# Performance work log

Hardware: AMD Instinct MI355X
Metric: run time of the kernel (lower is better)

The kernel has to match this reference:

```python
import jax, jax.numpy as jnp
import numpy as np
import math

D_MODEL = 1024
NUM_HEADS = 16
HEAD_DIM = D_MODEL // NUM_HEADS  # 64


def setup_inputs() -> dict:
    key = jax.random.key(0)
    ks = jax.random.split(key, 5)
    B, T = 4, 2048
    scale = 1.0 / math.sqrt(D_MODEL)
    return {
        "x": jax.random.normal(ks[0], (B, T, D_MODEL), dtype=jnp.float32),
        "wq": jax.random.normal(ks[1], (D_MODEL, D_MODEL), dtype=jnp.float32) * scale,
        "wk": jax.random.normal(ks[2], (D_MODEL, D_MODEL), dtype=jnp.float32) * scale,
        "wv": jax.random.normal(ks[3], (D_MODEL, D_MODEL), dtype=jnp.float32) * scale,
        "wo": jax.random.normal(ks[4], (D_MODEL, D_MODEL), dtype=jnp.float32) * scale,
    }


def reference(x, wq, wk, wv, wo):
    B, T, _ = x.shape
    H, Dk = NUM_HEADS, HEAD_DIM

    def split_heads(t):  # [B,T,D] -> [B,H,T,Dk]
        return t.reshape(B, T, H, Dk).transpose(0, 2, 1, 3)

    q = split_heads(x @ wq)
    k = split_heads(x @ wk)
    v = split_heads(x @ wv)

    # scaled QK^T: [B,H,T,T]
    scores = jnp.einsum("bhqd,bhkd->bhqk", q, k) / jnp.sqrt(jnp.float32(Dk))
    # causal mask: triu(ones, diag=0).T.bool() == lower-triangular incl. diagonal
    causal = jnp.tril(jnp.ones((T, T), dtype=bool))
    scores = jnp.where(causal, scores, -jnp.inf)
    attn = jax.nn.softmax(scores, axis=-1)

    out = jnp.einsum("bhqk,bhkd->bhqd", attn, v)  # [B,H,T,Dk]
    out = out.transpose(0, 2, 1, 3).reshape(B, T, H * Dk)
    return out @ wo
```

## Files before the change

kernel.cpp:

```cpp
#include <hip/hip_runtime.h>
#include <hip/hip_bf16.h>
#include <stdint.h>

typedef __attribute__((ext_vector_type(8))) short bf16x8;
typedef __attribute__((ext_vector_type(4))) float f32x4;
typedef __attribute__((ext_vector_type(4))) unsigned short u16x4;
typedef __attribute__((ext_vector_type(4))) float float4v;

#define MFMA16(a, b, c) __builtin_amdgcn_mfma_f32_16x16x32_bf16((a), (b), (c), 0, 0, 0)

__device__ __forceinline__ unsigned short f2bf(float f) {
  return __builtin_bit_cast(unsigned short, (__bf16)f);
}
__device__ __forceinline__ float m3(float a, float b, float c) {
  return fmaxf(fmaxf(a, b), c);
}

typedef const __attribute__((address_space(1))) void* gptr1_t;
typedef __attribute__((address_space(3))) void* lptr3_t;
__device__ __forceinline__ void gload16(const void* g, void* l) {
  __builtin_amdgcn_global_load_lds((gptr1_t)g, (lptr3_t)l, 16, 0, 0);
}

__global__ __launch_bounds__(256) void cvt_x_kernel(const float* __restrict__ in,
                                                    unsigned short* __restrict__ out) {
  int i = blockIdx.x * 256 + threadIdx.x;
  float4v f = ((const float4v*)in)[i];
  u16x4 o;
  o[0] = f2bf(f[0]); o[1] = f2bf(f[1]); o[2] = f2bf(f[2]); o[3] = f2bf(f[3]);
  ((u16x4*)out)[i] = o;
}

__global__ __launch_bounds__(256) void wt_cvt_kernel(const float* __restrict__ w0,
                                                     const float* __restrict__ w1,
                                                     const float* __restrict__ w2,
                                                     const float* __restrict__ w3,
                                                     unsigned short* __restrict__ out) {
  const float* in = blockIdx.z == 0 ? w0 : blockIdx.z == 1 ? w1 : blockIdx.z == 2 ? w2 : w3;
  unsigned short* o = out + (size_t)blockIdx.z * 1024 * 1024;
  __shared__ float tile[32][33];
  int tx = threadIdx.x & 31, ty = threadIdx.x >> 5;
  int c0 = blockIdx.x * 32, r0 = blockIdx.y * 32;
#pragma unroll
  for (int i = 0; i < 4; i++)
    tile[ty + 8 * i][tx] = in[(size_t)(r0 + ty + 8 * i) * 1024 + c0 + tx];
  __syncthreads();
#pragma unroll
  for (int i = 0; i < 4; i++)
    o[(size_t)(c0 + ty + 8 * i) * 1024 + r0 + tx] = f2bf(tile[tx][ty + 8 * i]);
}

template <bool OUTF32>
__global__ __launch_bounds__(256) void gemm128_kernel(
    const unsigned short* __restrict__ A,
    const unsigned short* __restrict__ B0, const unsigned short* __restrict__ B1,
    const unsigned short* __restrict__ B2,
    void* C0, void* C1, void* C2) {
  constexpr int K = 1024, N = 1024;
  const unsigned short* Bt = blockIdx.z == 0 ? B0 : blockIdx.z == 1 ? B1 : B2;
  void* Cv = blockIdx.z == 0 ? C0 : blockIdx.z == 1 ? C1 : C2;

  __shared__ unsigned short As[128 * 32];
  __shared__ unsigned short Bs[128 * 32];

  const int tid = threadIdx.x;
  const int w = tid >> 6, lane = tid & 63, l15 = lane & 15, l4 = lane >> 4;
  const int wm = w >> 1, wn = w & 1;
  const int m0 = blockIdx.x * 128, n0 = blockIdx.y * 128;

  f32x4 acc[4][4] = {};

  const int srow = w * 32 + (lane >> 2);
  const int scol = (lane & 3) * 8;
  const unsigned short* ga = A + (size_t)(m0 + srow) * K + scol;
  const unsigned short* gb = Bt + (size_t)(n0 + srow) * K + scol;
  char* lA = (char*)As + w * 2048;
  char* lB = (char*)Bs + w * 2048;

  for (int k0 = 0; k0 < K; k0 += 32) {
    __syncthreads();
    gload16(ga + k0, lA);
    gload16(ga + k0 + 16 * K, lA + 1024);
    gload16(gb + k0, lB);
    gload16(gb + k0 + 16 * K, lB + 1024);
    __syncthreads();

    bf16x8 af[4], bfr[4];
#pragma unroll
    for (int mi = 0; mi < 4; mi++)
      af[mi] = *(const bf16x8*)&As[(wm * 64 + mi * 16 + l15) * 32 + 8 * l4];
#pragma unroll
    for (int ni = 0; ni < 4; ni++)
      bfr[ni] = *(const bf16x8*)&Bs[(wn * 64 + ni * 16 + l15) * 32 + 8 * l4];
#pragma unroll
    for (int mi = 0; mi < 4; mi++)
#pragma unroll
      for (int ni = 0; ni < 4; ni++)
        acc[mi][ni] = MFMA16(af[mi], bfr[ni], acc[mi][ni]);
  }

#pragma unroll
  for (int mi = 0; mi < 4; mi++)
#pragma unroll
    for (int ni = 0; ni < 4; ni++)
#pragma unroll
      for (int r = 0; r < 4; r++) {
        int mg = m0 + wm * 64 + mi * 16 + 4 * l4 + r;
        int ng = n0 + wn * 64 + ni * 16 + l15;
        if (OUTF32)
          ((float*)Cv)[(size_t)mg * N + ng] = acc[mi][ni][r];
        else
          ((unsigned short*)Cv)[(size_t)mg * N + ng] = f2bf(acc[mi][ni][r]);
      }
}

__global__ __launch_bounds__(256) void gemm64_kernel(const unsigned short* __restrict__ A,
                                                     const unsigned short* __restrict__ Bt,
                                                     float* __restrict__ Cv) {
  constexpr int K = 1024, N = 1024;
  __shared__ unsigned short As[64 * 32];
  __shared__ unsigned short Bs[128 * 32];

  const int tid = threadIdx.x;
  const int w = tid >> 6, lane = tid & 63, l15 = lane & 15, l4 = lane >> 4;
  const int wm = w >> 1, wn = w & 1;
  const int m0 = blockIdx.x * 64, n0 = blockIdx.y * 128;

  f32x4 acc[2][4] = {};

  const int arow = w * 16 + (lane >> 2);
  const int brow = w * 32 + (lane >> 2);
  const int scol = (lane & 3) * 8;
  const unsigned short* ga = A + (size_t)(m0 + arow) * K + scol;
  const unsigned short* gb = Bt + (size_t)(n0 + brow) * K + scol;
  char* lA = (char*)As + w * 1024;
  char* lB = (char*)Bs + w * 2048;

  for (int k0 = 0; k0 < K; k0 += 32) {
    __syncthreads();
    gload16(ga + k0, lA);
    gload16(gb + k0, lB);
    gload16(gb + k0 + 16 * K, lB + 1024);
    __syncthreads();

    bf16x8 af[2], bfr[4];
#pragma unroll
    for (int mi = 0; mi < 2; mi++)
      af[mi] = *(const bf16x8*)&As[(wm * 32 + mi * 16 + l15) * 32 + 8 * l4];
#pragma unroll
    for (int ni = 0; ni < 4; ni++)
      bfr[ni] = *(const bf16x8*)&Bs[(wn * 64 + ni * 16 + l15) * 32 + 8 * l4];
#pragma unroll
    for (int mi = 0; mi < 2; mi++)
#pragma unroll
      for (int ni = 0; ni < 4; ni++)
        acc[mi][ni] = MFMA16(af[mi], bfr[ni], acc[mi][ni]);
  }

#pragma unroll
  for (int mi = 0; mi < 2; mi++)
#pragma unroll
    for (int ni = 0; ni < 4; ni++)
#pragma unroll
      for (int r = 0; r < 4; r++) {
        int mg = m0 + wm * 32 + mi * 16 + 4 * l4 + r;
        int ng = n0 + wn * 64 + ni * 16 + l15;
        Cv[(size_t)mg * N + ng] = acc[mi][ni][r];
      }
}

__global__ __launch_bounds__(256, 4) void attn_kernel(const unsigned short* __restrict__ Qb,
                                                      const unsigned short* __restrict__ Kb,
                                                      const unsigned short* __restrict__ Vb,
                                                      unsigned short* __restrict__ Ob) {
  const int bid = blockIdx.x;
  const int xcd = bid & 7, slot = bid >> 3;
  const int hb = xcd * 8 + (slot >> 4);
  const int p = slot & 15;
  const int h = hb & 15, bb = hb >> 4;

  const int tid = threadIdx.x, w = tid >> 6, lane = tid & 63, l15 = lane & 15, l4 = lane >> 4;

  __shared__ unsigned short K_lds[2][64 * 64];
  __shared__ unsigned short Vt_lds[2][64 * 64];
  __shared__ unsigned short P_lds[4][16 * 64];

  const size_t brow = (size_t)bb * 2048;
  const int qq = w * 16 + l15;
  const int sw = 8 * (l15 & 7);
  constexpr float C = 0.18033688f;
  const bf16x8 ones = {0x3F80, 0x3F80, 0x3F80, 0x3F80, 0x3F80, 0x3F80, 0x3F80, 0x3F80};

  const int qbA = p, qbB = 31 - p;
  const int lastB = qbB;

  bf16x8 qfA0, qfA1, qfB0, qfB1;
  {
    const unsigned short* qa = Qb + (brow + qbA * 64 + qq) * 1024 + h * 64 + 8 * l4;
    qfA0 = *(const bf16x8*)qa;
    qfA1 = *(const bf16x8*)(qa + 32);
    const unsigned short* qbp = Qb + (brow + qbB * 64 + qq) * 1024 + h * 64 + 8 * l4;
    qfB0 = *(const bf16x8*)qbp;
    qfB1 = *(const bf16x8*)(qbp + 32);
  }

  f32x4 oA[4] = {}, oB[4] = {};
  f32x4 lA4 = {0.f, 0.f, 0.f, 0.f}, lB4 = {0.f, 0.f, 0.f, 0.f};
  float mrA = -__builtin_inff(), mrB = -__builtin_inff();

  const int kcol = 8 * ((lane & 7) ^ ((lane >> 3) & 7));
  const unsigned short* gk = Kb + (brow + 8 * w + (lane >> 3)) * 1024 + h * 64 + kcol;
  const int vr0 = 2 * (tid >> 3);
  const int vsc = (tid & 7) * 8;
  const unsigned short* gv = Vb + (brow + vr0) * 1024 + h * 64 + vsc;

  auto vt_write = [&](int buf, const bf16x8& v0, const bf16x8& v1) {
#pragma unroll
    for (int j = 0; j < 8; j++) {
      const int d = vsc + j;
      const int msk = 8 * ((d ^ (d >> 3)) & 7);
      uint32_t pk = (uint32_t)(unsigned short)v0[j] |
                    ((uint32_t)(unsigned short)v1[j] << 16);
      *(uint32_t*)&Vt_lds[buf][d * 64 + (vr0 ^ msk)] = pk;
    }
  };

  auto tile_compute = [&](const unsigned short* Kc, const unsigned short* Vtc,
                          const bf16x8& q0f, const bf16x8& q1f, f32x4* oacc,
                          float& m_run, f32x4& lacc, bool diag) {
    f32x4 s[4];
    __builtin_amdgcn_s_setprio(1);
#pragma unroll
    for (int sub = 0; sub < 4; ++sub) {
      const unsigned short* kr0 = &Kc[(sub * 16 + l15) * 64 + ((8 * l4) ^ sw)];
      const unsigned short* kr1 = &Kc[(sub * 16 + l15) * 64 + ((32 + 8 * l4) ^ sw)];
      f32x4 z = {0.f, 0.f, 0.f, 0.f};
      z = MFMA16(*(const bf16x8*)kr0, q0f, z);
      z = MFMA16(*(const bf16x8*)kr1, q1f, z);
      s[sub] = z;
    }
    __builtin_amdgcn_s_setprio(0);

    if (diag) {
#pragma unroll
      for (int sub = 0; sub < 4; ++sub)
#pragma unroll
        for (int r4 = 0; r4 < 4; r4++) {
          const int kv_t = sub * 16 + 4 * l4 + r4;
          s[sub][r4] = (kv_t > qq) ? -__builtin_inff() : s[sub][r4];
        }
    }
    const float t0 = m3(s[0][0], s[0][1], s[0][2]);
    const float t1 = m3(s[0][3], s[1][0], s[1][1]);
    const float t2 = m3(s[1][2], s[1][3], s[2][0]);
    const float t3 = m3(s[2][1], s[2][2], s[2][3]);
    const float t4 = m3(s[3][0], s[3][1], s[3][2]);
    float mt = fmaxf(m3(t0, t1, t2), m3(t3, t4, s[3][3]));
    mt = fmaxf(mt, __shfl_xor(mt, 16));
    mt = fmaxf(mt, __shfl_xor(mt, 32));

    if (!__all(mt <= m_run + 44.3614f)) {
      const float m_new = fmaxf(m_run, mt);
      const float alpha = __builtin_amdgcn_exp2f((m_run - m_new) * C);
      const float ao0 = __shfl(alpha, 4 * l4 + 0);
      const float ao1 = __shfl(alpha, 4 * l4 + 1);
      const float ao2 = __shfl(alpha, 4 * l4 + 2);
      const float ao3 = __shfl(alpha, 4 * l4 + 3);
#pragma unroll
      for (int d = 0; d < 4; ++d) {
        oacc[d][0] *= ao0; oacc[d][1] *= ao1; oacc[d][2] *= ao2; oacc[d][3] *= ao3;
      }
      lacc[0] *= ao0; lacc[1] *= ao1; lacc[2] *= ao2; lacc[3] *= ao3;
      m_run = m_new;
    }
    const float mnc = m_run * C;

#pragma unroll
    for (int sub = 0; sub < 4; ++sub) {
      u16x4 pw;
#pragma unroll
      for (int r4 = 0; r4 < 4; r4++)
        pw[r4] = f2bf(__builtin_amdgcn_exp2f(__builtin_fmaf(s[sub][r4], C, -mnc)));
      *(u16x4*)&P_lds[w][l15 * 64 + ((sub * 16 + 4 * l4) ^ sw)] = pw;
    }

    const bf16x8 pf0 = *(const bf16x8*)&P_lds[w][l15 * 64 + ((8 * l4) ^ sw)];
    const bf16x8 pf1 = *(const bf16x8*)&P_lds[w][l15 * 64 + ((32 + 8 * l4) ^ sw)];
    __builtin_amdgcn_s_setprio(1);
#pragma unroll
    for (int d = 0; d < 4; ++d) {
      const int dd = d * 16 + l15;
      const int vm = 8 * ((dd ^ (dd >> 3)) & 7);
      const unsigned short* vp0 = &Vtc[dd * 64 + ((8 * l4) ^ vm)];
      const unsigned short* vp1 = &Vtc[dd * 64 + ((32 + 8 * l4) ^ vm)];
      oacc[d] = MFMA16(pf0, *(const bf16x8*)vp0, oacc[d]);
      oacc[d] = MFMA16(pf1, *(const bf16x8*)vp1, oacc[d]);
    }
    lacc = MFMA16(pf0, ones, lacc);
    lacc = MFMA16(pf1, ones, lacc);
    __builtin_amdgcn_s_setprio(0);
  };

  gload16(gk, (char*)K_lds[0] + w * 1024);
  gload16(gk + 32 * 1024, (char*)K_lds[0] + w * 1024 + 4096);
  {
    bf16x8 v0 = *(const bf16x8*)gv;
    bf16x8 v1 = *(const bf16x8*)(gv + 1024);
    vt_write(0, v0, v1);
  }
  __syncthreads();

  for (int kb = 0; kb <= lastB; ++kb) {
    const int cur = kb & 1, nxt = cur ^ 1;
    const bool pre = kb < lastB;
    bf16x8 pv0, pv1;
    if (pre) {
      const size_t off = (size_t)(kb + 1) * 64 * 1024;
      gload16(gk + off, (char*)K_lds[nxt] + w * 1024);
      gload16(gk + off + 32 * 1024, (char*)K_lds[nxt] + w * 1024 + 4096);
      pv0 = *(const bf16x8*)(gv + off);
      pv1 = *(const bf16x8*)(gv + off + 1024);
    }

    if (kb <= qbA)
      tile_compute(K_lds[cur], Vt_lds[cur], qfA0, qfA1, oA, mrA, lA4, kb == qbA);
    tile_compute(K_lds[cur], Vt_lds[cur], qfB0, qfB1, oB, mrB, lB4, kb == lastB);

    if (pre) vt_write(nxt, pv0, pv1);
    __syncthreads();
  }

  {
    const float li[4] = {1.0f / lA4[0], 1.0f / lA4[1], 1.0f / lA4[2], 1.0f / lA4[3]};
#pragma unroll
    for (int d = 0; d < 4; ++d)
#pragma unroll
      for (int r4 = 0; r4 < 4; r4++) {
        const size_t orow = brow + qbA * 64 + w * 16 + 4 * l4 + r4;
        Ob[orow * 1024 + h * 64 + d * 16 + l15] = f2bf(oA[d][r4] * li[r4]);
      }
  }
  {
    const float li[4] = {1.0f / lB4[0], 1.0f / lB4[1], 1.0f / lB4[2], 1.0f / lB4[3]};
#pragma unroll
    for (int d = 0; d < 4; ++d)
#pragma unroll
      for (int r4 = 0; r4 < 4; r4++) {
        const size_t orow = brow + qbB * 64 + w * 16 + 4 * l4 + r4;
        Ob[orow * 1024 + h * 64 + d * 16 + l15] = f2bf(oB[d][r4] * li[r4]);
      }
  }
}

extern "C" void kernel_launch(void* const* d_in, const int* in_sizes, int n_in,
                              void* d_out, int out_size, void* d_ws, size_t ws_size,
                              hipStream_t stream) {
  const float* x  = (const float*)d_in[0];
  const float* wq = (const float*)d_in[1];
  const float* wk = (const float*)d_in[2];
  const float* wv = (const float*)d_in[3];
  const float* wo = (const float*)d_in[4];

  char* ws = (char*)d_ws;
  unsigned short* Xb  = (unsigned short*)(ws);
  unsigned short* Wt  = (unsigned short*)(ws + (16u << 20));
  unsigned short* Wqt = Wt;
  unsigned short* Wkt = Wt + (1u << 20);
  unsigned short* Wvt = Wt + (2u << 20);
  unsigned short* Wot = Wt + (3u << 20);
  unsigned short* Qb  = (unsigned short*)(ws + (24u << 20));
  unsigned short* Kb  = (unsigned short*)(ws + (40u << 20));
  unsigned short* Vb  = (unsigned short*)(ws + (56u << 20));
  unsigned short* Ob  = Xb;

  cvt_x_kernel<<<8192, 256, 0, stream>>>(x, Xb);
  wt_cvt_kernel<<<dim3(32, 32, 4), 256, 0, stream>>>(wq, wk, wv, wo, Wt);
  gemm128_kernel<false><<<dim3(64, 8, 3), 256, 0, stream>>>(Xb, Wqt, Wkt, Wvt, Qb, Kb, Vb);
  attn_kernel<<<1024, 256, 0, stream>>>(Qb, Kb, Vb, Ob);
  gemm64_kernel<<<dim3(128, 8), 256, 0, stream>>>(Ob, Wot, (float*)d_out);
}
```

Before: 173.8 us.

## Interleave both query tiles per KV block sharing K/V fragment loads

Each wave's two query tiles (A and B) were computed as separate passes per key block, and each pass reloaded the K and V^T fragments from LDS. Now, when both tiles are active, the K fragments are loaded once and feed both QK^T MFMA chains interleaved. Softmax runs for each tile, then the V fragments are loaded once and used for both PV accumulations. This cuts LDS reads and gives the MFMA unit two independent dependency chains, at the cost of more live registers (two sets of scores and P fragments), which may reduce occupancy.

```diff
diff --git a/kernel.cpp b/kernel.cpp
--- a/kernel.cpp
+++ b/kernel.cpp
@@ -225,22 +225,8 @@
     }
   };
 
-  auto tile_compute = [&](const unsigned short* Kc, const unsigned short* Vtc,
-                          const bf16x8& q0f, const bf16x8& q1f, f32x4* oacc,
-                          float& m_run, f32x4& lacc, bool diag) {
-    f32x4 s[4];
-    __builtin_amdgcn_s_setprio(1);
-#pragma unroll
-    for (int sub = 0; sub < 4; ++sub) {
-      const unsigned short* kr0 = &Kc[(sub * 16 + l15) * 64 + ((8 * l4) ^ sw)];
-      const unsigned short* kr1 = &Kc[(sub * 16 + l15) * 64 + ((32 + 8 * l4) ^ sw)];
-      f32x4 z = {0.f, 0.f, 0.f, 0.f};
-      z = MFMA16(*(const bf16x8*)kr0, q0f, z);
-      z = MFMA16(*(const bf16x8*)kr1, q1f, z);
-      s[sub] = z;
-    }
-    __builtin_amdgcn_s_setprio(0);
-
+  auto smax = [&](f32x4 (&s)[4], float& m_run, f32x4* oacc, f32x4& lacc, bool diag,
+                  bf16x8& pf0, bf16x8& pf1) {
     if (diag) {
 #pragma unroll
       for (int sub = 0; sub < 4; ++sub)
@@ -283,22 +269,8 @@
         pw[r4] = f2bf(__builtin_amdgcn_exp2f(__builtin_fmaf(s[sub][r4], C, -mnc)));
       *(u16x4*)&P_lds[w][l15 * 64 + ((sub * 16 + 4 * l4) ^ sw)] = pw;
     }
-
-    const bf16x8 pf0 = *(const bf16x8*)&P_lds[w][l15 * 64 + ((8 * l4) ^ sw)];
-    const bf16x8 pf1 = *(const bf16x8*)&P_lds[w][l15 * 64 + ((32 + 8 * l4) ^ sw)];
-    __builtin_amdgcn_s_setprio(1);
-#pragma unroll
-    for (int d = 0; d < 4; ++d) {
-      const int dd = d * 16 + l15;
-      const int vm = 8 * ((dd ^ (dd >> 3)) & 7);
-      const unsigned short* vp0 = &Vtc[dd * 64 + ((8 * l4) ^ vm)];
-      const unsigned short* vp1 = &Vtc[dd * 64 + ((32 + 8 * l4) ^ vm)];
-      oacc[d] = MFMA16(pf0, *(const bf16x8*)vp0, oacc[d]);
-      oacc[d] = MFMA16(pf1, *(const bf16x8*)vp1, oacc[d]);
-    }
-    lacc = MFMA16(pf0, ones, lacc);
-    lacc = MFMA16(pf1, ones, lacc);
-    __builtin_amdgcn_s_setprio(0);
+    pf0 = *(const bf16x8*)&P_lds[w][l15 * 64 + ((8 * l4) ^ sw)];
+    pf1 = *(const bf16x8*)&P_lds[w][l15 * 64 + ((32 + 8 * l4) ^ sw)];
   };
 
   gload16(gk, (char*)K_lds[0] + w * 1024);
@@ -313,6 +285,8 @@
   for (int kb = 0; kb <= lastB; ++kb) {
     const int cur = kb & 1, nxt = cur ^ 1;
     const bool pre = kb < lastB;
+    const unsigned short* Kc = K_lds[cur];
+    const unsigned short* Vtc = Vt_lds[cur];
     bf16x8 pv0, pv1;
     if (pre) {
       const size_t off = (size_t)(kb + 1) * 64 * 1024;
@@ -322,9 +296,76 @@
       pv1 = *(const bf16x8*)(gv + off + 1024);
     }
 
-    if (kb <= qbA)
-      tile_compute(K_lds[cur], Vt_lds[cur], qfA0, qfA1, oA, mrA, lA4, kb == qbA);
-    tile_compute(K_lds[cur], Vt_lds[cur], qfB0, qfB1, oB, mrB, lB4, kb == lastB);
+    if (kb <= qbA) {
+      f32x4 sA[4], sB[4];
+      __builtin_amdgcn_s_setprio(1);
+#pragma unroll
+      for (int sub = 0; sub < 4; ++sub) {
+        const bf16x8 k0 = *(const bf16x8*)&Kc[(sub * 16 + l15) * 64 + ((8 * l4) ^ sw)];
+        const bf16x8 k1 = *(const bf16x8*)&Kc[(sub * 16 + l15) * 64 + ((32 + 8 * l4) ^ sw)];
+        f32x4 zA = {0.f, 0.f, 0.f, 0.f};
+        zA = MFMA16(k0, qfA0, zA);
+        zA = MFMA16(k1, qfA1, zA);
+        sA[sub] = zA;
+        f32x4 zB = {0.f, 0.f, 0.f, 0.f};
+        zB = MFMA16(k0, qfB0, zB);
+        zB = MFMA16(k1, qfB1, zB);
+        sB[sub] = zB;
+      }
+      __builtin_amdgcn_s_setprio(0);
+
+      bf16x8 pA0, pA1, pB0, pB1;
+      smax(sA, mrA, oA, lA4, kb == qbA, pA0, pA1);
+      smax(sB, mrB, oB, lB4, false, pB0, pB1);
+
+      __builtin_amdgcn_s_setprio(1);
+#pragma unroll
+      for (int d = 0; d < 4; ++d) {
+        const int dd = d * 16 + l15;
+        const int vm = 8 * ((dd ^ (dd >> 3)) & 7);
+        const bf16x8 v0 = *(const bf16x8*)&Vtc[dd * 64 + ((8 * l4) ^ vm)];
+        const bf16x8 v1 = *(const bf16x8*)&Vtc[dd * 64 + ((32 + 8 * l4) ^ vm)];
+        oA[d] = MFMA16(pA0, v0, oA[d]);
+        oA[d] = MFMA16(pA1, v1, oA[d]);
+        oB[d] = MFMA16(pB0, v0, oB[d]);
+        oB[d] = MFMA16(pB1, v1, oB[d]);
+      }
+      lA4 = MFMA16(pA0, ones, lA4);
+      lA4 = MFMA16(pA1, ones, lA4);
+      lB4 = MFMA16(pB0, ones, lB4);
+      lB4 = MFMA16(pB1, ones, lB4);
+      __builtin_amdgcn_s_setprio(0);
+    } else {
+      f32x4 sB[4];
+      __builtin_amdgcn_s_setprio(1);
+#pragma unroll
+      for (int sub = 0; sub < 4; ++sub) {
+        const bf16x8 k0 = *(const bf16x8*)&Kc[(sub * 16 + l15) * 64 + ((8 * l4) ^ sw)];
+        const bf16x8 k1 = *(const bf16x8*)&Kc[(sub * 16 + l15) * 64 + ((32 + 8 * l4) ^ sw)];
+        f32x4 zB = {0.f, 0.f, 0.f, 0.f};
+        zB = MFMA16(k0, qfB0, zB);
+        zB = MFMA16(k1, qfB1, zB);
+        sB[sub] = zB;
+      }
+      __builtin_amdgcn_s_setprio(0);
+
+      bf16x8 pB0, pB1;
+      smax(sB, mrB, oB, lB4, kb == lastB, pB0, pB1);
+
+      __builtin_amdgcn_s_setprio(1);
+#pragma unroll
+      for (int d = 0; d < 4; ++d) {
+        const int dd = d * 16 + l15;
+        const int vm = 8 * ((dd ^ (dd >> 3)) & 7);
+        const bf16x8 v0 = *(const bf16x8*)&Vtc[dd * 64 + ((8 * l4) ^ vm)];
+        const bf16x8 v1 = *(const bf16x8*)&Vtc[dd * 64 + ((32 + 8 * l4) ^ vm)];
+        oB[d] = MFMA16(pB0, v0, oB[d]);
+        oB[d] = MFMA16(pB1, v1, oB[d]);
+      }
+      lB4 = MFMA16(pB0, ones, lB4);
+      lB4 = MFMA16(pB1, ones, lB4);
+      __builtin_amdgcn_s_setprio(0);
+    }
 
     if (pre) vt_write(nxt, pv0, pv1);
     __syncthreads();
```

Measured after the change: 355.9 us. +104.7%, slower.

## Interleave both query tiles in attention loop to share K/V LDS fragment loads

Applied to the files above, without the earlier changes.

Replaces the per-query-tile lambda with macros that process tiles A and B together in the same phase. Each K and V fragment read from LDS now feeds the MFMAs of both tiles, and the softmax of both tiles sits between the QK and PV phases, which gives more independent MFMA work to interleave. Launch bounds drop from 4 to 3 waves-per-SIMD to make room for the extra live registers, which may reduce occupancy. The diagonal mask on B is only applied in the B-only branch, which is correct because B's diagonal block comes after A's last block.

```diff
diff --git a/kernel.cpp b/kernel.cpp
--- a/kernel.cpp
+++ b/kernel.cpp
@@ -169,7 +169,104 @@
       }
 }
 
-__global__ __launch_bounds__(256, 4) void attn_kernel(const unsigned short* __restrict__ Qb,
+
+#define QK_SUB2(SUB, SA, SB)                                                      \
+  {                                                                               \
+    const bf16x8 k0_ = *(const bf16x8*)&Kc[((SUB)*16 + l15) * 64 + ((8 * l4) ^ sw)]; \
+    const bf16x8 k1_ = *(const bf16x8*)&Kc[((SUB)*16 + l15) * 64 + ((32 + 8 * l4) ^ sw)]; \
+    f32x4 zA_ = {0.f, 0.f, 0.f, 0.f};                                             \
+    zA_ = MFMA16(k0_, qfA0, zA_);                                                 \
+    zA_ = MFMA16(k1_, qfA1, zA_);                                                 \
+    SA = zA_;                                                                     \
+    f32x4 zB_ = {0.f, 0.f, 0.f, 0.f};                                             \
+    zB_ = MFMA16(k0_, qfB0, zB_);                                                 \
+    zB_ = MFMA16(k1_, qfB1, zB_);                                                 \
+    SB = zB_;                                                                     \
+  }
+
+#define QK_SUB1(SUB, SB)                                                          \
+  {                                                                               \
+    const bf16x8 k0_ = *(const bf16x8*)&Kc[((SUB)*16 + l15) * 64 + ((8 * l4) ^ sw)]; \
+    const bf16x8 k1_ = *(const bf16x8*)&Kc[((SUB)*16 + l15) * 64 + ((32 + 8 * l4) ^ sw)]; \
+    f32x4 zB_ = {0.f, 0.f, 0.f, 0.f};                                             \
+    zB_ = MFMA16(k0_, qfB0, zB_);                                                 \
+    zB_ = MFMA16(k1_, qfB1, zB_);                                                 \
+    SB = zB_;                                                                     \
+  }
+
+#define SMAX(S0, S1, S2, S3, MR, OACC, LACC, DIAG, PF0, PF1)                      \
+  {                                                                               \
+    if (DIAG) {                                                                   \
+      _Pragma("unroll") for (int r4 = 0; r4 < 4; r4++) {                          \
+        if ( 0 + 4 * l4 + r4 > qq) S0[r4] = -__builtin_inff();                    \
+        if (16 + 4 * l4 + r4 > qq) S1[r4] = -__builtin_inff();                    \
+        if (32 + 4 * l4 + r4 > qq) S2[r4] = -__builtin_inff();                    \
+        if (48 + 4 * l4 + r4 > qq) S3[r4] = -__builtin_inff();                    \
+      }                                                                           \
+    }                                                                             \
+    const float t0_ = m3(S0[0], S0[1], S0[2]);                                    \
+    const float t1_ = m3(S0[3], S1[0], S1[1]);                                    \
+    const float t2_ = m3(S1[2], S1[3], S2[0]);                                    \
+    const float t3_ = m3(S2[1], S2[2], S2[3]);                                    \
+    const float t4_ = m3(S3[0], S3[1], S3[2]);                                    \
+    float mt_ = fmaxf(m3(t0_, t1_, t2_), m3(t3_, t4_, S3[3]));                    \
+    mt_ = fmaxf(mt_, __shfl_xor(mt_, 16));                                        \
+    mt_ = fmaxf(mt_, __shfl_xor(mt_, 32));                                        \
+    if (!__all(mt_ <= MR + 44.3614f)) {                                           \
+      const float mn_ = fmaxf(MR, mt_);                                           \
+      const float al_ = __builtin_amdgcn_exp2f((MR - mn_) * C);                   \
+      const float a0_ = __shfl(al_, 4 * l4 + 0);                                  \
+      const float a1_ = __shfl(al_, 4 * l4 + 1);                                  \
+      const float a2_ = __shfl(al_, 4 * l4 + 2);                                  \
+      const float a3_ = __shfl(al_, 4 * l4 + 3);                                  \
+      _Pragma("unroll") for (int d_ = 0; d_ < 4; ++d_) {                          \
+        OACC[d_][0] *= a0_; OACC[d_][1] *= a1_;                                   \
+        OACC[d_][2] *= a2_; OACC[d_][3] *= a3_;                                   \
+      }                                                                           \
+      LACC[0] *= a0_; LACC[1] *= a1_; LACC[2] *= a2_; LACC[3] *= a3_;             \
+      MR = mn_;                                                                   \
+    }                                                                             \
+    const float mnc_ = MR * C;                                                    \
+    u16x4 pw_;                                                                    \
+    _Pragma("unroll") for (int r4 = 0; r4 < 4; r4++)                              \
+      pw_[r4] = f2bf(__builtin_amdgcn_exp2f(__builtin_fmaf(S0[r4], C, -mnc_)));   \
+    *(u16x4*)&Pw[l15 * 64 + (( 0 + 4 * l4) ^ sw)] = pw_;                          \
+    _Pragma("unroll") for (int r4 = 0; r4 < 4; r4++)                              \
+      pw_[r4] = f2bf(__builtin_amdgcn_exp2f(__builtin_fmaf(S1[r4], C, -mnc_)));   \
+    *(u16x4*)&Pw[l15 * 64 + ((16 + 4 * l4) ^ sw)] = pw_;                          \
+    _Pragma("unroll") for (int r4 = 0; r4 < 4; r4++)                              \
+      pw_[r4] = f2bf(__builtin_amdgcn_exp2f(__builtin_fmaf(S2[r4], C, -mnc_)));   \
+    *(u16x4*)&Pw[l15 * 64 + ((32 + 4 * l4) ^ sw)] = pw_;                          \
+    _Pragma("unroll") for (int r4 = 0; r4 < 4; r4++)                              \
+      pw_[r4] = f2bf(__builtin_amdgcn_exp2f(__builtin_fmaf(S3[r4], C, -mnc_)));   \
+    *(u16x4*)&Pw[l15 * 64 + ((48 + 4 * l4) ^ sw)] = pw_;                          \
+    PF0 = *(const bf16x8*)&Pw[l15 * 64 + ((8 * l4) ^ sw)];                        \
+    PF1 = *(const bf16x8*)&Pw[l15 * 64 + ((32 + 8 * l4) ^ sw)];                   \
+  }
+
+#define PV_D2(DI)                                                                 \
+  {                                                                               \
+    const int dd_ = (DI) * 16 + l15;                                              \
+    const int vm_ = 8 * ((dd_ ^ (dd_ >> 3)) & 7);                                 \
+    const bf16x8 v0_ = *(const bf16x8*)&Vtc[dd_ * 64 + ((8 * l4) ^ vm_)];         \
+    const bf16x8 v1_ = *(const bf16x8*)&Vtc[dd_ * 64 + ((32 + 8 * l4) ^ vm_)];    \
+    oA[DI] = MFMA16(pA0, v0_, oA[DI]);                                            \
+    oA[DI] = MFMA16(pA1, v1_, oA[DI]);                                            \
+    oB[DI] = MFMA16(pB0, v0_, oB[DI]);                                            \
+    oB[DI] = MFMA16(pB1, v1_, oB[DI]);                                            \
+  }
+
+#define PV_D1(DI)                                                                 \
+  {                                                                               \
+    const int dd_ = (DI) * 16 + l15;                                              \
+    const int vm_ = 8 * ((dd_ ^ (dd_ >> 3)) & 7);                                 \
+    const bf16x8 v0_ = *(const bf16x8*)&Vtc[dd_ * 64 + ((8 * l4) ^ vm_)];         \
+    const bf16x8 v1_ = *(const bf16x8*)&Vtc[dd_ * 64 + ((32 + 8 * l4) ^ vm_)];    \
+    oB[DI] = MFMA16(pB0, v0_, oB[DI]);                                            \
+    oB[DI] = MFMA16(pB1, v1_, oB[DI]);                                            \
+  }
+
+__global__ __launch_bounds__(256, 3) void attn_kernel(const unsigned short* __restrict__ Qb,
                                                       const unsigned short* __restrict__ Kb,
                                                       const unsigned short* __restrict__ Vb,
                                                       unsigned short* __restrict__ Ob) {
@@ -190,6 +287,7 @@
   const int sw = 8 * (l15 & 7);
   constexpr float C = 0.18033688f;
   const bf16x8 ones = {0x3F80, 0x3F80, 0x3F80, 0x3F80, 0x3F80, 0x3F80, 0x3F80, 0x3F80};
+  unsigned short* Pw = &P_lds[w][0];
 
   const int qbA = p, qbB = 31 - p;
   const int lastB = qbB;
@@ -225,82 +323,6 @@
     }
   };
 
-  auto tile_compute = [&](const unsigned short* Kc, const unsigned short* Vtc,
-                          const bf16x8& q0f, const bf16x8& q1f, f32x4* oacc,
-                          float& m_run, f32x4& lacc, bool diag) {
-    f32x4 s[4];
-    __builtin_amdgcn_s_setprio(1);
-#pragma unroll
-    for (int sub = 0; sub < 4; ++sub) {
-      const unsigned short* kr0 = &Kc[(sub * 16 + l15) * 64 + ((8 * l4) ^ sw)];
-      const unsigned short* kr1 = &Kc[(sub * 16 + l15) * 64 + ((32 + 8 * l4) ^ sw)];
-      f32x4 z = {0.f, 0.f, 0.f, 0.f};
-      z = MFMA16(*(const bf16x8*)kr0, q0f, z);
-      z = MFMA16(*(const bf16x8*)kr1, q1f, z);
-      s[sub] = z;
-    }
-    __builtin_amdgcn_s_setprio(0);
-
-    if (diag) {
-#pragma unroll
-      for (int sub = 0; sub < 4; ++sub)
-#pragma unroll
-        for (int r4 = 0; r4 < 4; r4++) {
-          const int kv_t = sub * 16 + 4 * l4 + r4;
-          s[sub][r4] = (kv_t > qq) ? -__builtin_inff() : s[sub][r4];
-        }
-    }
-    const float t0 = m3(s[0][0], s[0][1], s[0][2]);
-    const float t1 = m3(s[0][3], s[1][0], s[1][1]);
-    const float t2 = m3(s[1][2], s[1][3], s[2][0]);
-    const float t3 = m3(s[2][1], s[2][2], s[2][3]);
-    const float t4 = m3(s[3][0], s[3][1], s[3][2]);
-    float mt = fmaxf(m3(t0, t1, t2), m3(t3, t4, s[3][3]));
-    mt = fmaxf(mt, __shfl_xor(mt, 16));
-    mt = fmaxf(mt, __shfl_xor(mt, 32));
-
-    if (!__all(mt <= m_run + 44.3614f)) {
-      const float m_new = fmaxf(m_run, mt);
-      const float alpha = __builtin_amdgcn_exp2f((m_run - m_new) * C);
-      const float ao0 = __shfl(alpha, 4 * l4 + 0);
-      const float ao1 = __shfl(alpha, 4 * l4 + 1);
-      const float ao2 = __shfl(alpha, 4 * l4 + 2);
-      const float ao3 = __shfl(alpha, 4 * l4 + 3);
-#pragma unroll
-      for (int d = 0; d < 4; ++d) {
-        oacc[d][0] *= ao0; oacc[d][1] *= ao1; oacc[d][2] *= ao2; oacc[d][3] *= ao3;
-      }
-      lacc[0] *= ao0; lacc[1] *= ao1; lacc[2] *= ao2; lacc[3] *= ao3;
-      m_run = m_new;
-    }
-    const float mnc = m_run * C;
-
-#pragma unroll
-    for (int sub = 0; sub < 4; ++sub) {
-      u16x4 pw;
-#pragma unroll
-      for (int r4 = 0; r4 < 4; r4++)
-        pw[r4] = f2bf(__builtin_amdgcn_exp2f(__builtin_fmaf(s[sub][r4], C, -mnc)));
-      *(u16x4*)&P_lds[w][l15 * 64 + ((sub * 16 + 4 * l4) ^ sw)] = pw;
-    }
-
-    const bf16x8 pf0 = *(const bf16x8*)&P_lds[w][l15 * 64 + ((8 * l4) ^ sw)];
-    const bf16x8 pf1 = *(const bf16x8*)&P_lds[w][l15 * 64 + ((32 + 8 * l4) ^ sw)];
-    __builtin_amdgcn_s_setprio(1);
-#pragma unroll
-    for (int d = 0; d < 4; ++d) {
-      const int dd = d * 16 + l15;
-      const int vm = 8 * ((dd ^ (dd >> 3)) & 7);
-      const unsigned short* vp0 = &Vtc[dd * 64 + ((8 * l4) ^ vm)];
-      const unsigned short* vp1 = &Vtc[dd * 64 + ((32 + 8 * l4) ^ vm)];
-      oacc[d] = MFMA16(pf0, *(const bf16x8*)vp0, oacc[d]);
-      oacc[d] = MFMA16(pf1, *(const bf16x8*)vp1, oacc[d]);
-    }
-    lacc = MFMA16(pf0, ones, lacc);
-    lacc = MFMA16(pf1, ones, lacc);
-    __builtin_amdgcn_s_setprio(0);
-  };
-
   gload16(gk, (char*)K_lds[0] + w * 1024);
   gload16(gk + 32 * 1024, (char*)K_lds[0] + w * 1024 + 4096);
   {
@@ -313,6 +335,8 @@
   for (int kb = 0; kb <= lastB; ++kb) {
     const int cur = kb & 1, nxt = cur ^ 1;
     const bool pre = kb < lastB;
+    const unsigned short* Kc = K_lds[cur];
+    const unsigned short* Vtc = Vt_lds[cur];
     bf16x8 pv0, pv1;
     if (pre) {
       const size_t off = (size_t)(kb + 1) * 64 * 1024;
@@ -322,9 +346,46 @@
       pv1 = *(const bf16x8*)(gv + off + 1024);
     }
 
-    if (kb <= qbA)
-      tile_compute(K_lds[cur], Vt_lds[cur], qfA0, qfA1, oA, mrA, lA4, kb == qbA);
-    tile_compute(K_lds[cur], Vt_lds[cur], qfB0, qfB1, oB, mrB, lB4, kb == lastB);
+    if (kb <= qbA) {
+      f32x4 sA0, sA1, sA2, sA3, sB0, sB1, sB2, sB3;
+      __builtin_amdgcn_s_setprio(1);
+      QK_SUB2(0, sA0, sB0)
+      QK_SUB2(1, sA1, sB1)
+      QK_SUB2(2, sA2, sB2)
+      QK_SUB2(3, sA3, sB3)
+      __builtin_amdgcn_s_setprio(0);
+
+      bf16x8 pA0, pA1, pB0, pB1;
+      const bool diagA = (kb == qbA);
+      SMAX(sA0, sA1, sA2, sA3, mrA, oA, lA4, diagA, pA0, pA1)
+      SMAX(sB0, sB1, sB2, sB3, mrB, oB, lB4, false, pB0, pB1)
+
+      __builtin_amdgcn_s_setprio(1);
+      PV_D2(0) PV_D2(1) PV_D2(2) PV_D2(3)
+      lA4 = MFMA16(pA0, ones, lA4);
+      lA4 = MFMA16(pA1, ones, lA4);
+      lB4 = MFMA16(pB0, ones, lB4);
+      lB4 = MFMA16(pB1, ones, lB4);
+      __builtin_amdgcn_s_setprio(0);
+    } else {
+      f32x4 sB0, sB1, sB2, sB3;
+      __builtin_amdgcn_s_setprio(1);
+      QK_SUB1(0, sB0)
+      QK_SUB1(1, sB1)
+      QK_SUB1(2, sB2)
+      QK_SUB1(3, sB3)
+      __builtin_amdgcn_s_setprio(0);
+
+      bf16x8 pB0, pB1;
+      const bool diagB = (kb == lastB);
+      SMAX(sB0, sB1, sB2, sB3, mrB, oB, lB4, diagB, pB0, pB1)
+
+      __builtin_amdgcn_s_setprio(1);
+      PV_D1(0) PV_D1(1) PV_D1(2) PV_D1(3)
+      lB4 = MFMA16(pB0, ones, lB4);
+      lB4 = MFMA16(pB1, ones, lB4);
+      __builtin_amdgcn_s_setprio(0);
+    }
 
     if (pre) vt_write(nxt, pv0, pv1);
     __syncthreads();
```

New measurement: 209.4 us. +20.4%, slower.

## Merge paired query tiles into one 32x32 MFMA attention pass with register P

Applied to the files above, without the earlier changes.

Rewrites the attention inner loop so each wave handles its 16 rows from the early query block and its 16 rows from the late block together as one 32-row tile, using 32x32x16 bf16 MFMAs instead of two separate 16x16 passes. The P matrix is exchanged across half-waves with shuffles instead of a round trip through LDS, and the row sum is accumulated in registers rather than with an extra MFMA against ones. The output is staged through LDS for coalesced 16-byte global stores. The cost is that rows of the early block run through every KV tile after their diagonal and are masked as dead, so those MFMAs are wasted work.

```diff
diff --git a/kernel.cpp b/kernel.cpp
--- a/kernel.cpp
+++ b/kernel.cpp
@@ -4,13 +4,19 @@
 
 typedef __attribute__((ext_vector_type(8))) short bf16x8;
 typedef __attribute__((ext_vector_type(4))) float f32x4;
+typedef __attribute__((ext_vector_type(16))) float f32x16;
 typedef __attribute__((ext_vector_type(4))) unsigned short u16x4;
+typedef __attribute__((ext_vector_type(4))) unsigned int u32x4;
 typedef __attribute__((ext_vector_type(4))) float float4v;
 
 #define MFMA16(a, b, c) __builtin_amdgcn_mfma_f32_16x16x32_bf16((a), (b), (c), 0, 0, 0)
+#define MFMA32(a, b, c) __builtin_amdgcn_mfma_f32_32x32x16_bf16((a), (b), (c), 0, 0, 0)
 
 __device__ __forceinline__ unsigned short f2bf(float f) {
   return __builtin_bit_cast(unsigned short, (__bf16)f);
+}
+__device__ __forceinline__ uint32_t pk2(float a, float b) {
+  return (uint32_t)f2bf(a) | ((uint32_t)f2bf(b) << 16);
 }
 __device__ __forceinline__ float m3(float a, float b, float c) {
   return fmaxf(fmaxf(a, b), c);
@@ -169,6 +175,14 @@
       }
 }
 
+#define QK_KC(KCC, QF)                                                               \
+  {                                                                                  \
+    const bf16x8 kf0_ = *(const bf16x8*)&Kc[l31 * 64 + (((KCC)*16 + 8 * hf) ^ ksw)]; \
+    const bf16x8 kf1_ = *(const bf16x8*)&Kc[(l31 + 32) * 64 + (((KCC)*16 + 8 * hf) ^ ksw)]; \
+    s0 = MFMA32(kf0_, QF, s0);                                                       \
+    s1 = MFMA32(kf1_, QF, s1);                                                       \
+  }
+
 __global__ __launch_bounds__(256, 4) void attn_kernel(const unsigned short* __restrict__ Qb,
                                                       const unsigned short* __restrict__ Kb,
                                                       const unsigned short* __restrict__ Vb,
@@ -177,128 +191,50 @@
   const int xcd = bid & 7, slot = bid >> 3;
   const int hb = xcd * 8 + (slot >> 4);
   const int p = slot & 15;
-  const int h = hb & 15, bb = hb >> 4;
-
-  const int tid = threadIdx.x, w = tid >> 6, lane = tid & 63, l15 = lane & 15, l4 = lane >> 4;
+  const int hh = hb & 15, bb = hb >> 4;
+
+  const int tid = threadIdx.x, w = tid >> 6, lane = tid & 63;
+  const int l31 = lane & 31, hf = lane >> 5;
 
   __shared__ unsigned short K_lds[2][64 * 64];
   __shared__ unsigned short Vt_lds[2][64 * 64];
-  __shared__ unsigned short P_lds[4][16 * 64];
 
   const size_t brow = (size_t)bb * 2048;
-  const int qq = w * 16 + l15;
-  const int sw = 8 * (l15 & 7);
   constexpr float C = 0.18033688f;
-  const bf16x8 ones = {0x3F80, 0x3F80, 0x3F80, 0x3F80, 0x3F80, 0x3F80, 0x3F80, 0x3F80};
-
-  const int qbA = p, qbB = 31 - p;
-  const int lastB = qbB;
-
-  bf16x8 qfA0, qfA1, qfB0, qfB1;
+  const float NEGINF = -__builtin_inff();
+  const int qbA = p, qbB = 31 - p, lastB = qbB;
+  const int ksw = 8 * (l31 & 7);
+
+  const int q_g = (l31 < 16) ? (qbA * 64 + w * 16 + l31) : (qbB * 64 + w * 16 + (l31 - 16));
+
+  bf16x8 qf0, qf1, qf2, qf3;
   {
-    const unsigned short* qa = Qb + (brow + qbA * 64 + qq) * 1024 + h * 64 + 8 * l4;
-    qfA0 = *(const bf16x8*)qa;
-    qfA1 = *(const bf16x8*)(qa + 32);
-    const unsigned short* qbp = Qb + (brow + qbB * 64 + qq) * 1024 + h * 64 + 8 * l4;
-    qfB0 = *(const bf16x8*)qbp;
-    qfB1 = *(const bf16x8*)(qbp + 32);
-  }
-
-  f32x4 oA[4] = {}, oB[4] = {};
-  f32x4 lA4 = {0.f, 0.f, 0.f, 0.f}, lB4 = {0.f, 0.f, 0.f, 0.f};
-  float mrA = -__builtin_inff(), mrB = -__builtin_inff();
+    const unsigned short* qp = Qb + (brow + q_g) * 1024 + hh * 64 + 8 * hf;
+    qf0 = *(const bf16x8*)qp;
+    qf1 = *(const bf16x8*)(qp + 16);
+    qf2 = *(const bf16x8*)(qp + 32);
+    qf3 = *(const bf16x8*)(qp + 48);
+  }
+
+  f32x16 oO0 = {0,0,0,0,0,0,0,0,0,0,0,0,0,0,0,0};
+  f32x16 oO1 = {0,0,0,0,0,0,0,0,0,0,0,0,0,0,0,0};
+  float m_run = NEGINF, l_run = 0.0f;
 
   const int kcol = 8 * ((lane & 7) ^ ((lane >> 3) & 7));
-  const unsigned short* gk = Kb + (brow + 8 * w + (lane >> 3)) * 1024 + h * 64 + kcol;
+  const unsigned short* gk = Kb + (brow + 8 * w + (lane >> 3)) * 1024 + hh * 64 + kcol;
   const int vr0 = 2 * (tid >> 3);
   const int vsc = (tid & 7) * 8;
-  const unsigned short* gv = Vb + (brow + vr0) * 1024 + h * 64 + vsc;
+  const unsigned short* gv = Vb + (brow + vr0) * 1024 + hh * 64 + vsc;
 
   auto vt_write = [&](int buf, const bf16x8& v0, const bf16x8& v1) {
 #pragma unroll
     for (int j = 0; j < 8; j++) {
       const int d = vsc + j;
       const int msk = 8 * ((d ^ (d >> 3)) & 7);
-      uint32_t pk = (uint32_t)(unsigned short)v0[j] |
-                    ((uint32_t)(unsigned short)v1[j] << 16);
-      *(uint32_t*)&Vt_lds[buf][d * 64 + (vr0 ^ msk)] = pk;
-    }
-  };
-
-  auto tile_compute = [&](const unsigned short* Kc, const unsigned short* Vtc,
-                          const bf16x8& q0f, const bf16x8& q1f, f32x4* oacc,
-                          float& m_run, f32x4& lacc, bool diag) {
-    f32x4 s[4];
-    __builtin_amdgcn_s_setprio(1);
-#pragma unroll
-    for (int sub = 0; sub < 4; ++sub) {
-      const unsigned short* kr0 = &Kc[(sub * 16 + l15) * 64 + ((8 * l4) ^ sw)];
-      const unsigned short* kr1 = &Kc[(sub * 16 + l15) * 64 + ((32 + 8 * l4) ^ sw)];
-      f32x4 z = {0.f, 0.f, 0.f, 0.f};
-      z = MFMA16(*(const bf16x8*)kr0, q0f, z);
-      z = MFMA16(*(const bf16x8*)kr1, q1f, z);
-      s[sub] = z;
-    }
-    __builtin_amdgcn_s_setprio(0);
-
-    if (diag) {
-#pragma unroll
-      for (int sub = 0; sub < 4; ++sub)
-#pragma unroll
-        for (int r4 = 0; r4 < 4; r4++) {
-          const int kv_t = sub * 16 + 4 * l4 + r4;
-          s[sub][r4] = (kv_t > qq) ? -__builtin_inff() : s[sub][r4];
-        }
-    }
-    const float t0 = m3(s[0][0], s[0][1], s[0][2]);
-    const float t1 = m3(s[0][3], s[1][0], s[1][1]);
-    const float t2 = m3(s[1][2], s[1][3], s[2][0]);
-    const float t3 = m3(s[2][1], s[2][2], s[2][3]);
-    const float t4 = m3(s[3][0], s[3][1], s[3][2]);
-    float mt = fmaxf(m3(t0, t1, t2), m3(t3, t4, s[3][3]));
-    mt = fmaxf(mt, __shfl_xor(mt, 16));
-    mt = fmaxf(mt, __shfl_xor(mt, 32));
-
-    if (!__all(mt <= m_run + 44.3614f)) {
-      const float m_new = fmaxf(m_run, mt);
-      const float alpha = __builtin_amdgcn_exp2f((m_run - m_new) * C);
-      const float ao0 = __shfl(alpha, 4 * l4 + 0);
-      const float ao1 = __shfl(alpha, 4 * l4 + 1);
-      const float ao2 = __shfl(alpha, 4 * l4 + 2);
-      const float ao3 = __shfl(alpha, 4 * l4 + 3);
-#pragma unroll
-      for (int d = 0; d < 4; ++d) {
-        oacc[d][0] *= ao0; oacc[d][1] *= ao1; oacc[d][2] *= ao2; oacc[d][3] *= ao3;
-      }
-      lacc[0] *= ao0; lacc[1] *= ao1; lacc[2] *= ao2; lacc[3] *= ao3;
-      m_run = m_new;
-    }
-    const float mnc = m_run * C;
-
-#pragma unroll
-    for (int sub = 0; sub < 4; ++sub) {
-      u16x4 pw;
-#pragma unroll
-      for (int r4 = 0; r4 < 4; r4++)
-        pw[r4] = f2bf(__builtin_amdgcn_exp2f(__builtin_fmaf(s[sub][r4], C, -mnc)));
-      *(u16x4*)&P_lds[w][l15 * 64 + ((sub * 16 + 4 * l4) ^ sw)] = pw;
-    }
-
-    const bf16x8 pf0 = *(const bf16x8*)&P_lds[w][l15 * 64 + ((8 * l4) ^ sw)];
-    const bf16x8 pf1 = *(const bf16x8*)&P_lds[w][l15 * 64 + ((32 + 8 * l4) ^ sw)];
-    __builtin_amdgcn_s_setprio(1);
-#pragma unroll
-    for (int d = 0; d < 4; ++d) {
-      const int dd = d * 16 + l15;
-      const int vm = 8 * ((dd ^ (dd >> 3)) & 7);
-      const unsigned short* vp0 = &Vtc[dd * 64 + ((8 * l4) ^ vm)];
-      const unsigned short* vp1 = &Vtc[dd * 64 + ((32 + 8 * l4) ^ vm)];
-      oacc[d] = MFMA16(pf0, *(const bf16x8*)vp0, oacc[d]);
-      oacc[d] = MFMA16(pf1, *(const bf16x8*)vp1, oacc[d]);
-    }
-    lacc = MFMA16(pf0, ones, lacc);
-    lacc = MFMA16(pf1, ones, lacc);
-    __builtin_amdgcn_s_setprio(0);
+      uint32_t pkv = (uint32_t)(unsigned short)v0[j] |
+                     ((uint32_t)(unsigned short)v1[j] << 16);
+      *(uint32_t*)&Vt_lds[buf][d * 64 + (vr0 ^ msk)] = pkv;
+    }
   };
 
   gload16(gk, (char*)K_lds[0] + w * 1024);
@@ -310,9 +246,14 @@
   }
   __syncthreads();
 
+  const int vm0 = 8 * ((l31 ^ (l31 >> 3)) & 7);
+  const int vm1 = 8 * (((l31 + 32) ^ ((l31 + 32) >> 3)) & 7);
+
   for (int kb = 0; kb <= lastB; ++kb) {
     const int cur = kb & 1, nxt = cur ^ 1;
     const bool pre = kb < lastB;
+    const unsigned short* Kc = K_lds[cur];
+    const unsigned short* Vtc = Vt_lds[cur];
     bf16x8 pv0, pv1;
     if (pre) {
       const size_t off = (size_t)(kb + 1) * 64 * 1024;
@@ -322,33 +263,125 @@
       pv1 = *(const bf16x8*)(gv + off + 1024);
     }
 
-    if (kb <= qbA)
-      tile_compute(K_lds[cur], Vt_lds[cur], qfA0, qfA1, oA, mrA, lA4, kb == qbA);
-    tile_compute(K_lds[cur], Vt_lds[cur], qfB0, qfB1, oB, mrB, lB4, kb == lastB);
+    f32x16 s0 = {0,0,0,0,0,0,0,0,0,0,0,0,0,0,0,0};
+    f32x16 s1 = {0,0,0,0,0,0,0,0,0,0,0,0,0,0,0,0};
+    __builtin_amdgcn_s_setprio(1);
+    QK_KC(0, qf0) QK_KC(1, qf1) QK_KC(2, qf2) QK_KC(3, qf3)
+    __builtin_amdgcn_s_setprio(0);
+
+    if (kb == qbA || kb == lastB) {
+      const int kv0 = kb * 64;
+#pragma unroll
+      for (int r = 0; r < 16; r++) {
+        const int kvl = (r & 3) + 8 * (r >> 2) + 4 * hf;
+        if (kv0 + kvl > q_g) s0[r] = NEGINF;
+        if (kv0 + kvl + 32 > q_g) s1[r] = NEGINF;
+      }
+    }
+    const bool dead = (l31 < 16) && (kb > qbA);
+
+    float mt;
+    {
+      float a0 = m3(s0[0], s0[1], s0[2]),  a1 = m3(s0[3], s0[4], s0[5]);
+      float a2 = m3(s0[6], s0[7], s0[8]),  a3 = m3(s0[9], s0[10], s0[11]);
+      float a4 = m3(s0[12], s0[13], s0[14]);
+      float b0 = m3(s1[0], s1[1], s1[2]),  b1 = m3(s1[3], s1[4], s1[5]);
+      float b2 = m3(s1[6], s1[7], s1[8]),  b3 = m3(s1[9], s1[10], s1[11]);
+      float b4 = m3(s1[12], s1[13], s1[14]);
+      float t0 = m3(a0, a1, a2), t1 = m3(a3, a4, s0[15]);
+      float t2 = m3(b0, b1, b2), t3 = m3(b3, b4, s1[15]);
+      mt = fmaxf(fmaxf(t0, t1), fmaxf(t2, t3));
+    }
+    mt = dead ? NEGINF : mt;
+    mt = fmaxf(mt, __shfl_xor(mt, 32));
+
+    float alpha = 1.0f;
+    bool doresc = false;
+    if (!__all(mt <= m_run + 44.3614f)) {
+      const float m_new = fmaxf(m_run, mt);
+      alpha = __builtin_amdgcn_exp2f((m_run - m_new) * C);
+      m_run = m_new;
+      doresc = true;
+    }
+    const float mnc = dead ? __builtin_inff() : m_run * C;
+
+    float lt = 0.0f;
+    uint32_t pw[16];
+#pragma unroll
+    for (int rp = 0; rp < 8; rp++) {
+      float e0 = __builtin_amdgcn_exp2f(__builtin_fmaf(s0[2 * rp], C, -mnc));
+      float e1 = __builtin_amdgcn_exp2f(__builtin_fmaf(s0[2 * rp + 1], C, -mnc));
+      lt += e0 + e1;
+      pw[rp] = pk2(e0, e1);
+      float f0 = __builtin_amdgcn_exp2f(__builtin_fmaf(s1[2 * rp], C, -mnc));
+      float f1 = __builtin_amdgcn_exp2f(__builtin_fmaf(s1[2 * rp + 1], C, -mnc));
+      lt += f0 + f1;
+      pw[8 + rp] = pk2(f0, f1);
+    }
+    lt += __shfl_xor(lt, 32);
+    if (doresc) {
+#pragma unroll
+      for (int r = 0; r < 16; r++) { oO0[r] *= alpha; oO1[r] *= alpha; }
+      l_run *= alpha;
+    }
+    l_run += lt;
+
+    const bool hi = (hf == 1);
+    bf16x8 pf0k, pf1k, pf2k, pf3k;
+#pragma unroll
+    for (int kc = 0; kc < 4; kc++) {
+      const int base = 8 * (kc >> 1) + 4 * (kc & 1);
+      const uint32_t wA = pw[base], wB = pw[base + 1], wC = pw[base + 2], wD = pw[base + 3];
+      const uint32_t sA = hi ? wA : wC;
+      const uint32_t sB = hi ? wB : wD;
+      const uint32_t r1 = __shfl_xor(sA, 32);
+      const uint32_t r2 = __shfl_xor(sB, 32);
+      u32x4 fw;
+      fw[0] = hi ? r1 : wA;
+      fw[1] = hi ? r2 : wB;
+      fw[2] = hi ? wC : r1;
+      fw[3] = hi ? wD : r2;
+      const bf16x8 pf = __builtin_bit_cast(bf16x8, fw);
+      if (kc == 0) pf0k = pf; else if (kc == 1) pf1k = pf;
+      else if (kc == 2) pf2k = pf; else pf3k = pf;
+    }
+
+    __builtin_amdgcn_s_setprio(1);
+#pragma unroll
+    for (int kc = 0; kc < 4; kc++) {
+      const bf16x8 pf = kc == 0 ? pf0k : kc == 1 ? pf1k : kc == 2 ? pf2k : pf3k;
+      const bf16x8 vf0 = *(const bf16x8*)&Vtc[l31 * 64 + ((16 * kc + 8 * hf) ^ vm0)];
+      const bf16x8 vf1 = *(const bf16x8*)&Vtc[(l31 + 32) * 64 + ((16 * kc + 8 * hf) ^ vm1)];
+      oO0 = MFMA32(vf0, pf, oO0);
+      oO1 = MFMA32(vf1, pf, oO1);
+    }
+    __builtin_amdgcn_s_setprio(0);
 
     if (pre) vt_write(nxt, pv0, pv1);
     __syncthreads();
   }
 
+  const float li = 1.0f / l_run;
+  unsigned short* tb = &K_lds[0][0] + w * 2048;
+#pragma unroll
+  for (int rp = 0; rp < 8; rp++) {
+    const int dd0 = ((2 * rp) & 3) + 8 * (rp >> 1) + 4 * hf;
+    *(uint32_t*)&tb[l31 * 64 + (dd0 ^ (8 * (l31 & 7)))] =
+        pk2(oO0[2 * rp] * li, oO0[2 * rp + 1] * li);
+    const int dd1 = dd0 + 32;
+    *(uint32_t*)&tb[l31 * 64 + (dd1 ^ (8 * (l31 & 7)))] =
+        pk2(oO1[2 * rp] * li, oO1[2 * rp + 1] * li);
+  }
   {
-    const float li[4] = {1.0f / lA4[0], 1.0f / lA4[1], 1.0f / lA4[2], 1.0f / lA4[3]};
-#pragma unroll
-    for (int d = 0; d < 4; ++d)
-#pragma unroll
-      for (int r4 = 0; r4 < 4; r4++) {
-        const size_t orow = brow + qbA * 64 + w * 16 + 4 * l4 + r4;
-        Ob[orow * 1024 + h * 64 + d * 16 + l15] = f2bf(oA[d][r4] * li[r4]);
-      }
-  }
-  {
-    const float li[4] = {1.0f / lB4[0], 1.0f / lB4[1], 1.0f / lB4[2], 1.0f / lB4[3]};
-#pragma unroll
-    for (int d = 0; d < 4; ++d)
-#pragma unroll
-      for (int r4 = 0; r4 < 4; r4++) {
-        const size_t orow = brow + qbB * 64 + w * 16 + 4 * l4 + r4;
-        Ob[orow * 1024 + h * 64 + d * 16 + l15] = f2bf(oB[d][r4] * li[r4]);
-      }
+    const int rq = lane >> 1;
+    const int q_out = (rq < 16) ? (qbA * 64 + w * 16 + rq) : (qbB * 64 + w * 16 + (rq - 16));
+    const int dbase = (lane & 1) * 32;
+#pragma unroll
+    for (int c = 0; c < 4; c++) {
+      const int dcol = dbase + 8 * c;
+      bf16x8 ov = *(const bf16x8*)&tb[rq * 64 + (dcol ^ (8 * (rq & 7)))];
+      *(bf16x8*)&Ob[(brow + q_out) * 1024 + hh * 64 + dcol] = ov;
+    }
   }
 }
 
```

Result: slower. 214.2 us (+23.2%).
